# Kernel optimization log

Hardware: AMD Instinct MI355X
Metric: run time of the kernel (lower is better)

The kernel has to match this reference:

```python
import jax, jax.numpy as jnp
import numpy as np

EMBED_DIM = 1024
NUM_HEADS = 16
HEAD_DIM = EMBED_DIM // NUM_HEADS
SCALE = HEAD_DIM ** -0.5
BATCH, SEQ = 2, 2048


def setup_inputs() -> dict:
    key = jax.random.key(0)
    k1, k2, k3 = jax.random.split(key, 3)
    # Xavier-uniform-like init scales
    s_qkv = (6.0 / (3 * EMBED_DIM + EMBED_DIM)) ** 0.5
    s_out = (6.0 / (2 * EMBED_DIM)) ** 0.5
    return {
        "x": jax.random.normal(k1, (BATCH, SEQ, EMBED_DIM), dtype=jnp.float32),
        "w_qkv": jax.random.uniform(k2, (3 * EMBED_DIM, EMBED_DIM), jnp.float32, -s_qkv, s_qkv),
        "w_out": jax.random.uniform(k3, (EMBED_DIM, EMBED_DIM), jnp.float32, -s_out, s_out),
        "bias_qkv": jnp.zeros((3 * EMBED_DIM,), jnp.float32),
        "bias_out": jnp.zeros((EMBED_DIM,), jnp.float32),
    }


def reference(x, w_qkv, w_out, bias_qkv, bias_out):
    B, S, E = x.shape
    H, D = NUM_HEADS, HEAD_DIM
    # Fused QKV projection: [B,S,3E]
    qkv = jnp.einsum('bse,fe->bsf', x, w_qkv) + bias_qkv
    q, k, v = jnp.split(qkv, 3, axis=-1)
    # [B,H,S,D]
    q = q.reshape(B, S, H, D).transpose(0, 2, 1, 3)
    k = k.reshape(B, S, H, D).transpose(0, 2, 1, 3)
    v = v.reshape(B, S, H, D).transpose(0, 2, 1, 3)
    # Scaled dot-product attention (non-causal, no mask)
    scores = jnp.einsum('bhqd,bhkd->bhqk', q, k) * SCALE
    attn = jax.nn.softmax(scores, axis=-1)
    ctx = jnp.einsum('bhqk,bhkd->bhqd', attn, v)
    ctx = ctx.transpose(0, 2, 1, 3).reshape(B, S, E)
    # Output projection
    return jnp.einsum('bse,fe->bsf', ctx, w_out) + bias_out
```

## Files before the change

kernel.cpp:

```cpp
#include <hip/hip_runtime.h>
#include <stdint.h>

#define B_ 2
#define S_ 2048
#define E_ 1024
#define H_ 16
#define D_ 64
#define QSCALE_ 0.18033688011112042f

typedef __attribute__((ext_vector_type(4))) short short4_t;
typedef __attribute__((ext_vector_type(8))) short short8;
typedef __attribute__((ext_vector_type(2))) float f32x2;
typedef __attribute__((ext_vector_type(4))) float f32x4;
typedef __attribute__((ext_vector_type(16))) float f32x16;
typedef unsigned int u32;

__device__ __forceinline__ unsigned short f2bf(float x) {
    union { float f; u32 u; } v; v.f = x;
    u32 r = v.u + 0x7fffu + ((v.u >> 16) & 1u);
    return (unsigned short)(r >> 16);
}
__device__ __forceinline__ u32 fbits(float x) {
    union { float f; u32 u; } v; v.f = x; return v.u;
}
__device__ __forceinline__ u32 pkbf(float lo, float hi) {
    return __builtin_amdgcn_perm(fbits(hi), fbits(lo), 0x07060302u);
}

__device__ __forceinline__ f32x4 mfma16(short8 a, short8 b, f32x4 c) {
    return __builtin_amdgcn_mfma_f32_16x16x32_bf16(a, b, c, 0, 0, 0);
}
__device__ __forceinline__ f32x16 mfma32(short8 a, short8 b, f32x16 c) {
    return __builtin_amdgcn_mfma_f32_32x32x16_bf16(a, b, c, 0, 0, 0);
}

__device__ __forceinline__ void gld16(const unsigned short* g, unsigned short* l) {
    __builtin_amdgcn_global_load_lds(
        (const __attribute__((address_space(1))) u32*)g,
        (__attribute__((address_space(3))) u32*)l, 16, 0, 0);
}

__global__ __launch_bounds__(256) void cvt_kernel(
    const float* __restrict__ x, const float* __restrict__ wq,
    const float* __restrict__ wo,
    unsigned short* __restrict__ xb, unsigned short* __restrict__ wqb,
    unsigned short* __restrict__ wob)
{
    const long i8 = ((long)blockIdx.x * 256 + threadIdx.x) * 8;
    const float* src; unsigned short* dst; long off;
    if (i8 < 4194304)      { src = x;  dst = xb;  off = i8; }
    else if (i8 < 7340032) { src = wq; dst = wqb; off = i8 - 4194304; }
    else                   { src = wo; dst = wob; off = i8 - 7340032; }
    f32x4 a = *(const f32x4*)(src + off);
    f32x4 b = *(const f32x4*)(src + off + 4);
    short8 o;
    o[0] = (short)f2bf(a[0]); o[1] = (short)f2bf(a[1]);
    o[2] = (short)f2bf(a[2]); o[3] = (short)f2bf(a[3]);
    o[4] = (short)f2bf(b[0]); o[5] = (short)f2bf(b[1]);
    o[6] = (short)f2bf(b[2]); o[7] = (short)f2bf(b[3]);
    *(short8*)(dst + off) = o;
}

__global__ __launch_bounds__(256) void qkv_gemm_kernel(
    const unsigned short* __restrict__ x, const unsigned short* __restrict__ w,
    const float* __restrict__ bias,
    unsigned short* __restrict__ Qg, unsigned short* __restrict__ Kg,
    unsigned short* __restrict__ Vtg)
{
    __shared__ __attribute__((aligned(16))) unsigned char smem[16896];
    __shared__ float biass[128];
    unsigned short* As = (unsigned short*)smem;
    unsigned short* Bs = (unsigned short*)(smem + 8192);
    float* Tr = (float*)smem;

    const int t = threadIdx.x;
    const int m0 = blockIdx.x * 128;
    const int n0 = blockIdx.y * 128;
    const int lane = t & 63;
    const int wv = t >> 6;
    const int g = lane >> 4;
    const int l15 = lane & 15;
    const int wm = (wv >> 1) * 64;
    const int wn = (wv & 1) * 64;
    const int rloc = lane >> 2;
    const int cg = (lane & 3) ^ ((lane >> 3) & 3);
    const int rsw = (g ^ ((l15 >> 1) & 3)) * 8;

    if (t < 128) biass[t] = bias[n0 + t];

    f32x4 acc[4][4];
#pragma unroll
    for (int i = 0; i < 4; ++i)
#pragma unroll
        for (int j = 0; j < 4; ++j)
            acc[i][j] = (f32x4){0.f, 0.f, 0.f, 0.f};

    for (int kt = 0; kt < E_; kt += 32) {
        __syncthreads();
#pragma unroll
        for (int j = 0; j < 2; ++j) {
            const int rb = 32 * wv + 16 * j;
            gld16(x + (m0 + rb + rloc) * E_ + kt + cg * 8, &As[rb * 32]);
            gld16(w + (n0 + rb + rloc) * E_ + kt + cg * 8, &Bs[rb * 32]);
        }
        __syncthreads();

        short8 af[4], bf[4];
#pragma unroll
        for (int mt = 0; mt < 4; ++mt)
            af[mt] = *(const short8*)&As[(wm + mt * 16 + l15) * 32 + rsw];
#pragma unroll
        for (int nt = 0; nt < 4; ++nt)
            bf[nt] = *(const short8*)&Bs[(wn + nt * 16 + l15) * 32 + rsw];
#pragma unroll
        for (int mt = 0; mt < 4; ++mt)
#pragma unroll
            for (int nt = 0; nt < 4; ++nt)
                acc[mt][nt] = mfma16(af[mt], bf[nt], acc[mt][nt]);
    }

    if (n0 < 2048) {
#pragma unroll
        for (int mt = 0; mt < 4; ++mt) {
#pragma unroll
            for (int nt = 0; nt < 4; ++nt) {
                const int col = n0 + wn + nt * 16 + l15;
                const int which = col >> 10;
                const int cr = col & 1023;
                const int h = cr >> 6;
                const int d = cr & 63;
                const float bia = biass[col - n0];
#pragma unroll
                for (int i = 0; i < 4; ++i) {
                    const int row = m0 + wm + mt * 16 + g * 4 + i;
                    const int bb = row >> 11;
                    const int s = row & 2047;
                    const int bh = bb * H_ + h;
                    const float v = acc[mt][nt][i] + bia;
                    if (which == 0)
                        Qg[(bh * S_ + s) * D_ + d] = f2bf(v * QSCALE_);
                    else
                        Kg[(bh * S_ + s) * D_ + d] = f2bf(v);
                }
            }
        }
    } else {
        const int bb = m0 >> 11;
        const int s0 = m0 & 2047;
        const int dth = t >> 3;
        const int sc = t & 7;
#pragma unroll
        for (int sl = 0; sl < 4; ++sl) {
            __syncthreads();
            if ((wv & 1) == (sl >> 1)) {
#pragma unroll
                for (int q = 0; q < 2; ++q) {
                    const int nt = (sl & 1) * 2 + q;
                    const float bia = biass[wn + nt * 16 + l15];
                    const int dloc = q * 16 + l15;
#pragma unroll
                    for (int mt = 0; mt < 4; ++mt)
#pragma unroll
                        for (int i = 0; i < 4; ++i)
                            Tr[(wm + mt * 16 + g * 4 + i) * 33 + dloc] =
                                acc[mt][nt][i] + bia;
                }
            }
            __syncthreads();
            const int dglob = (n0 - 2048) + sl * 32 + dth;
            const int h = dglob >> 6;
            const int dd = dglob & 63;
            unsigned short* dst =
                Vtg + ((long)(bb * H_ + h) * D_ + dd) * S_ + s0 + sc * 16;
            short8 o0, o1;
#pragma unroll
            for (int j = 0; j < 8; ++j)
                o0[j] = (short)f2bf(Tr[(sc * 16 + j) * 33 + dth]);
#pragma unroll
            for (int j = 0; j < 8; ++j)
                o1[j] = (short)f2bf(Tr[(sc * 16 + 8 + j) * 33 + dth]);
            *(short8*)dst = o0;
            *(short8*)(dst + 8) = o1;
        }
    }
}

__global__ __launch_bounds__(128) void attn_kernel(
    const unsigned short* __restrict__ Qg, const unsigned short* __restrict__ Kg,
    const unsigned short* __restrict__ Vtg, unsigned short* __restrict__ ctx)
{
    __shared__ __attribute__((aligned(16))) unsigned short Ks[2][64 * 64];
    __shared__ __attribute__((aligned(16))) unsigned short Vs[2][64 * 64];
    __shared__ float lsumbuf[64];

    const int t = threadIdx.x;
    const int qb = blockIdx.x;
    const int bh = blockIdx.y;
    const int bb = bh >> 4;
    const int hh = bh & 15;
    const int lane = t & 63;
    const int wv = t >> 6;
    const int l31 = lane & 31;
    const int hf = lane >> 5;
    const int rloc = lane >> 3;
    const int cg = (lane & 7) ^ ((lane >> 3) & 7);
    const int sw = (l31 & 7);

    const int qrow0 = qb * 64 + wv * 32;
    short8 qa[4];
#pragma unroll
    for (int kc = 0; kc < 4; ++kc)
        qa[kc] = *(const short8*)(Qg + (bh * S_ + qrow0 + l31) * D_ + kc * 16 + hf * 8);

    const unsigned short* kp = Kg + (bh * S_ + 32 * wv + rloc) * D_ + cg * 8;
    const unsigned short* vp0 = Vtg + ((bh * D_ + 32 * wv + 0  + rloc) * S_) + cg * 8;
    const unsigned short* vp1 = Vtg + ((bh * D_ + 32 * wv + 8  + rloc) * S_) + cg * 8;
    const unsigned short* vp2 = Vtg + ((bh * D_ + 32 * wv + 16 + rloc) * S_) + cg * 8;
    const unsigned short* vp3 = Vtg + ((bh * D_ + 32 * wv + 24 + rloc) * S_) + cg * 8;

    f32x16 O[2];
    f32x2 lsum2 = (f32x2){0.f, 0.f};
#pragma unroll
    for (int r = 0; r < 16; ++r) { O[0][r] = 0.f; O[1][r] = 0.f; }

    auto stage = [&](int bufi) {
        unsigned short* kd = &Ks[bufi][(32 * wv) * 64];
        unsigned short* vd = &Vs[bufi][(32 * wv) * 64];
        gld16(kp,        kd);
        gld16(kp + 512,  kd + 512);
        gld16(kp + 1024, kd + 1024);
        gld16(kp + 1536, kd + 1536);
        gld16(vp0, vd);
        gld16(vp1, vd + 512);
        gld16(vp2, vd + 1024);
        gld16(vp3, vd + 1536);
    };
    auto advance = [&]() {
        kp += 64 * D_;
        vp0 += 64; vp1 += 64; vp2 += 64; vp3 += 64;
    };

    stage(0);
    advance();

    for (int kb = 0; kb < S_ / 64; ++kb) {
        __syncthreads();
        if (kb + 1 < S_ / 64) { stage((kb + 1) & 1); advance(); }
        const unsigned short* ks = Ks[kb & 1];
        const unsigned short* vs = Vs[kb & 1];

        f32x16 st[2];
#pragma unroll
        for (int kt = 0; kt < 2; ++kt) {
            f32x16 s;
#pragma unroll
            for (int r = 0; r < 16; ++r) s[r] = 0.f;
#pragma unroll
            for (int kc = 0; kc < 4; ++kc) {
                short8 kf = *(const short8*)&ks[(kt * 32 + l31) * 64 + ((2 * kc + hf) ^ sw) * 8];
                s = mfma32(kf, qa[kc], s);
            }
            st[kt] = s;
        }

#pragma unroll
        for (int kt = 0; kt < 2; ++kt) {
#pragma unroll
            for (int cp = 0; cp < 2; ++cp) {
                float p[8];
#pragma unroll
                for (int j = 0; j < 8; ++j)
                    p[j] = __builtin_amdgcn_exp2f(st[kt][8 * cp + j]);
                lsum2 += (f32x2){p[0], p[1]};
                lsum2 += (f32x2){p[2], p[3]};
                lsum2 += (f32x2){p[4], p[5]};
                lsum2 += (f32x2){p[6], p[7]};
                union { short8 s8; u32 u[4]; } pa;
                pa.u[0] = pkbf(p[0], p[1]);
                pa.u[1] = pkbf(p[2], p[3]);
                pa.u[2] = pkbf(p[4], p[5]);
                pa.u[3] = pkbf(p[6], p[7]);
                const int c0 = ((4 * kt + 2 * cp) ^ sw) * 8 + 4 * hf;
                const int c1 = ((4 * kt + 2 * cp + 1) ^ sw) * 8 + 4 * hf;
#pragma unroll
                for (int dt = 0; dt < 2; ++dt) {
                    short4_t v0 = *(const short4_t*)&vs[(dt * 32 + l31) * 64 + c0];
                    short4_t v1 = *(const short4_t*)&vs[(dt * 32 + l31) * 64 + c1];
                    short8 vb = __builtin_shufflevector(v0, v1, 0, 1, 2, 3, 4, 5, 6, 7);
                    O[dt] = mfma32(pa.s8, vb, O[dt]);
                }
            }
        }
    }

    float lsum = lsum2[0] + lsum2[1];
    lsum += __shfl_xor(lsum, 32);
    if (hf == 0) lsumbuf[wv * 32 + l31] = lsum;
    float inv[16];
#pragma unroll
    for (int r = 0; r < 16; ++r) {
        const int ql = wv * 32 + 4 * hf + (r & 3) + 8 * (r >> 2);
        inv[r] = 1.0f / lsumbuf[ql];
    }

#pragma unroll
    for (int dt = 0; dt < 2; ++dt)
#pragma unroll
        for (int r = 0; r < 16; ++r) {
            const int ql = wv * 32 + 4 * hf + (r & 3) + 8 * (r >> 2);
            const int s = qb * 64 + ql;
            ctx[(bb * S_ + s) * E_ + hh * D_ + dt * 32 + l31] = f2bf(O[dt][r] * inv[r]);
        }
}

__global__ __launch_bounds__(256) void out_gemm_kernel(
    const unsigned short* __restrict__ ctxg, const unsigned short* __restrict__ w,
    const float* __restrict__ bias, float* __restrict__ out)
{
    __shared__ __attribute__((aligned(16))) unsigned short As[128 * 32];
    __shared__ __attribute__((aligned(16))) unsigned short Bs[64 * 32];
    __shared__ float biass[64];

    const int t = threadIdx.x;
    const int m0 = blockIdx.x * 128;
    const int n0 = blockIdx.y * 64;
    const int lane = t & 63;
    const int wv = t >> 6;
    const int g = lane >> 4;
    const int l15 = lane & 15;
    const int wm = (wv >> 1) * 64;
    const int wn = (wv & 1) * 32;
    const int rloc = lane >> 2;
    const int cg = (lane & 3) ^ ((lane >> 3) & 3);
    const int rsw = (g ^ ((l15 >> 1) & 3)) * 8;

    if (t < 64) biass[t] = bias[n0 + t];

    f32x4 acc[4][2];
#pragma unroll
    for (int i = 0; i < 4; ++i)
#pragma unroll
        for (int j = 0; j < 2; ++j)
            acc[i][j] = (f32x4){0.f, 0.f, 0.f, 0.f};

    for (int kt = 0; kt < E_; kt += 32) {
        __syncthreads();
#pragma unroll
        for (int j = 0; j < 2; ++j) {
            const int rb = 32 * wv + 16 * j;
            gld16(ctxg + (m0 + rb + rloc) * E_ + kt + cg * 8, &As[rb * 32]);
        }
        {
            const int rb = 16 * wv;
            gld16(w + (n0 + rb + rloc) * E_ + kt + cg * 8, &Bs[rb * 32]);
        }
        __syncthreads();

        short8 af[4], bf[2];
#pragma unroll
        for (int mt = 0; mt < 4; ++mt)
            af[mt] = *(const short8*)&As[(wm + mt * 16 + l15) * 32 + rsw];
#pragma unroll
        for (int nt = 0; nt < 2; ++nt)
            bf[nt] = *(const short8*)&Bs[(wn + nt * 16 + l15) * 32 + rsw];
#pragma unroll
        for (int mt = 0; mt < 4; ++mt)
#pragma unroll
            for (int nt = 0; nt < 2; ++nt)
                acc[mt][nt] = mfma16(af[mt], bf[nt], acc[mt][nt]);
    }

#pragma unroll
    for (int mt = 0; mt < 4; ++mt) {
#pragma unroll
        for (int nt = 0; nt < 2; ++nt) {
            const int col = n0 + wn + nt * 16 + l15;
            const float bia = biass[col - n0];
#pragma unroll
            for (int i = 0; i < 4; ++i) {
                const int row = m0 + wm + mt * 16 + g * 4 + i;
                out[row * E_ + col] = acc[mt][nt][i] + bia;
            }
        }
    }
}

extern "C" void kernel_launch(void* const* d_in, const int* in_sizes, int n_in,
                              void* d_out, int out_size, void* d_ws, size_t ws_size,
                              hipStream_t stream) {
    const float* x    = (const float*)d_in[0];
    const float* wqkv = (const float*)d_in[1];
    const float* wout = (const float*)d_in[2];
    const float* bqkv = (const float*)d_in[3];
    const float* bout = (const float*)d_in[4];

    unsigned short* Q   = (unsigned short*)d_ws;
    unsigned short* K   = Q + 4194304;
    unsigned short* Vt  = K + 4194304;
    unsigned short* ctx = Vt + 4194304;
    unsigned short* xb  = ctx;
    unsigned short* wqb = ctx + 4194304;
    unsigned short* wob = wqb + 3145728;

    cvt_kernel<<<4096, 256, 0, stream>>>(x, wqkv, wout, xb, wqb, wob);
    qkv_gemm_kernel<<<dim3(32, 24), 256, 0, stream>>>(xb, wqb, bqkv, Q, K, Vt);
    attn_kernel<<<dim3(32, 32), 128, 0, stream>>>(Q, K, Vt, ctx);
    out_gemm_kernel<<<dim3(32, 16), 256, 0, stream>>>(ctx, wob, bout, (float*)d_out);
}
```

Before: 188.2 us.

## Use one wave per attention block computing 64 query rows with shared K/V fragments

The attention kernel now runs one 64-lane wave per block instead of two waves, and that wave handles both 32-row query halves. Each K and V fragment read from LDS is reused for two query tiles, which halves LDS fragment reads per MFMA, and V is read as a single short8 instead of two short4 loads. The cost is roughly double the registers per wave (two O accumulators and two Q sets) and fewer waves per CU to hide latency. Each stage now issues 16 global-to-LDS loads per lane, and a waitcnt(0) is added before every barrier. The QKV transpose store reorders element packing in a way that looks like it changes the output layout.

```diff
diff --git a/kernel.cpp b/kernel.cpp
--- a/kernel.cpp
+++ b/kernel.cpp
@@ -8,9 +8,7 @@
 #define D_ 64
 #define QSCALE_ 0.18033688011112042f
 
-typedef __attribute__((ext_vector_type(4))) short short4_t;
 typedef __attribute__((ext_vector_type(8))) short short8;
-typedef __attribute__((ext_vector_type(2))) float f32x2;
 typedef __attribute__((ext_vector_type(4))) float f32x4;
 typedef __attribute__((ext_vector_type(16))) float f32x16;
 typedef unsigned int u32;
@@ -174,18 +172,19 @@
                 Vtg + ((long)(bb * H_ + h) * D_ + dd) * S_ + s0 + sc * 16;
             short8 o0, o1;
 #pragma unroll
-            for (int j = 0; j < 8; ++j)
-                o0[j] = (short)f2bf(Tr[(sc * 16 + j) * 33 + dth]);
-#pragma unroll
-            for (int j = 0; j < 8; ++j)
-                o1[j] = (short)f2bf(Tr[(sc * 16 + 8 + j) * 33 + dth]);
+            for (int j = 0; j < 4; ++j) {
+                o0[j]     = (short)f2bf(Tr[(sc * 16 + j)      * 33 + dth]);
+                o0[4 + j] = (short)f2bf(Tr[(sc * 16 + 8 + j)  * 33 + dth]);
+                o1[j]     = (short)f2bf(Tr[(sc * 16 + 4 + j)  * 33 + dth]);
+                o1[4 + j] = (short)f2bf(Tr[(sc * 16 + 12 + j) * 33 + dth]);
+            }
             *(short8*)dst = o0;
             *(short8*)(dst + 8) = o1;
         }
     }
 }
 
-__global__ __launch_bounds__(128) void attn_kernel(
+__global__ __launch_bounds__(64, 1) void attn_kernel(
     const unsigned short* __restrict__ Qg, const unsigned short* __restrict__ Kg,
     const unsigned short* __restrict__ Vtg, unsigned short* __restrict__ ctx)
 {
@@ -193,124 +192,130 @@
     __shared__ __attribute__((aligned(16))) unsigned short Vs[2][64 * 64];
     __shared__ float lsumbuf[64];
 
-    const int t = threadIdx.x;
+    const int lane = threadIdx.x;
     const int qb = blockIdx.x;
     const int bh = blockIdx.y;
     const int bb = bh >> 4;
     const int hh = bh & 15;
-    const int lane = t & 63;
-    const int wv = t >> 6;
     const int l31 = lane & 31;
     const int hf = lane >> 5;
     const int rloc = lane >> 3;
     const int cg = (lane & 7) ^ ((lane >> 3) & 7);
-    const int sw = (l31 & 7);
-
-    const int qrow0 = qb * 64 + wv * 32;
-    short8 qa[4];
-#pragma unroll
-    for (int kc = 0; kc < 4; ++kc)
-        qa[kc] = *(const short8*)(Qg + (bh * S_ + qrow0 + l31) * D_ + kc * 16 + hf * 8);
-
-    const unsigned short* kp = Kg + (bh * S_ + 32 * wv + rloc) * D_ + cg * 8;
-    const unsigned short* vp0 = Vtg + ((bh * D_ + 32 * wv + 0  + rloc) * S_) + cg * 8;
-    const unsigned short* vp1 = Vtg + ((bh * D_ + 32 * wv + 8  + rloc) * S_) + cg * 8;
-    const unsigned short* vp2 = Vtg + ((bh * D_ + 32 * wv + 16 + rloc) * S_) + cg * 8;
-    const unsigned short* vp3 = Vtg + ((bh * D_ + 32 * wv + 24 + rloc) * S_) + cg * 8;
-
-    f32x16 O[2];
-    f32x2 lsum2 = (f32x2){0.f, 0.f};
-#pragma unroll
-    for (int r = 0; r < 16; ++r) { O[0][r] = 0.f; O[1][r] = 0.f; }
-
-    auto stage = [&](int bufi) {
-        unsigned short* kd = &Ks[bufi][(32 * wv) * 64];
-        unsigned short* vd = &Vs[bufi][(32 * wv) * 64];
-        gld16(kp,        kd);
-        gld16(kp + 512,  kd + 512);
-        gld16(kp + 1024, kd + 1024);
-        gld16(kp + 1536, kd + 1536);
-        gld16(vp0, vd);
-        gld16(vp1, vd + 512);
-        gld16(vp2, vd + 1024);
-        gld16(vp3, vd + 1536);
+    const int sw = l31 & 7;
+
+    short8 qa[2][4];
+#pragma unroll
+    for (int qh = 0; qh < 2; ++qh)
+#pragma unroll
+        for (int kc = 0; kc < 4; ++kc)
+            qa[qh][kc] = *(const short8*)(
+                Qg + (bh * S_ + qb * 64 + qh * 32 + l31) * D_ + kc * 16 + hf * 8);
+
+    f32x16 O[2][2];
+    float lsum[2] = {0.f, 0.f};
+#pragma unroll
+    for (int qh = 0; qh < 2; ++qh)
+#pragma unroll
+        for (int dt = 0; dt < 2; ++dt)
+#pragma unroll
+            for (int r = 0; r < 16; ++r) O[qh][dt][r] = 0.f;
+
+    auto stage = [&](int kb2, int bufi) {
+#pragma unroll
+        for (int i = 0; i < 8; ++i)
+            gld16(Kg + (bh * S_ + kb2 * 64 + i * 8 + rloc) * D_ + cg * 8,
+                  &Ks[bufi][i * 512]);
+#pragma unroll
+        for (int i = 0; i < 8; ++i)
+            gld16(Vtg + (bh * D_ + i * 8 + rloc) * S_ + kb2 * 64 + cg * 8,
+                  &Vs[bufi][i * 512]);
     };
-    auto advance = [&]() {
-        kp += 64 * D_;
-        vp0 += 64; vp1 += 64; vp2 += 64; vp3 += 64;
-    };
-
-    stage(0);
-    advance();
+
+    stage(0, 0);
 
     for (int kb = 0; kb < S_ / 64; ++kb) {
+        __builtin_amdgcn_s_waitcnt(0);
         __syncthreads();
-        if (kb + 1 < S_ / 64) { stage((kb + 1) & 1); advance(); }
+        if (kb + 1 < S_ / 64) stage(kb + 1, (kb + 1) & 1);
         const unsigned short* ks = Ks[kb & 1];
         const unsigned short* vs = Vs[kb & 1];
 
-        f32x16 st[2];
+        f32x16 st[2][2];
 #pragma unroll
         for (int kt = 0; kt < 2; ++kt) {
-            f32x16 s;
-#pragma unroll
-            for (int r = 0; r < 16; ++r) s[r] = 0.f;
-#pragma unroll
-            for (int kc = 0; kc < 4; ++kc) {
-                short8 kf = *(const short8*)&ks[(kt * 32 + l31) * 64 + ((2 * kc + hf) ^ sw) * 8];
-                s = mfma32(kf, qa[kc], s);
-            }
-            st[kt] = s;
+            short8 kf[4];
+#pragma unroll
+            for (int kc = 0; kc < 4; ++kc)
+                kf[kc] = *(const short8*)&ks[(kt * 32 + l31) * 64 + ((2 * kc + hf) ^ sw) * 8];
+#pragma unroll
+            for (int qh = 0; qh < 2; ++qh) {
+                f32x16 s;
+#pragma unroll
+                for (int r = 0; r < 16; ++r) s[r] = 0.f;
+#pragma unroll
+                for (int kc = 0; kc < 4; ++kc)
+                    s = mfma32(kf[kc], qa[qh][kc], s);
+                st[kt][qh] = s;
+            }
         }
 
 #pragma unroll
         for (int kt = 0; kt < 2; ++kt) {
 #pragma unroll
             for (int cp = 0; cp < 2; ++cp) {
-                float p[8];
-#pragma unroll
-                for (int j = 0; j < 8; ++j)
-                    p[j] = __builtin_amdgcn_exp2f(st[kt][8 * cp + j]);
-                lsum2 += (f32x2){p[0], p[1]};
-                lsum2 += (f32x2){p[2], p[3]};
-                lsum2 += (f32x2){p[4], p[5]};
-                lsum2 += (f32x2){p[6], p[7]};
-                union { short8 s8; u32 u[4]; } pa;
-                pa.u[0] = pkbf(p[0], p[1]);
-                pa.u[1] = pkbf(p[2], p[3]);
-                pa.u[2] = pkbf(p[4], p[5]);
-                pa.u[3] = pkbf(p[6], p[7]);
-                const int c0 = ((4 * kt + 2 * cp) ^ sw) * 8 + 4 * hf;
-                const int c1 = ((4 * kt + 2 * cp + 1) ^ sw) * 8 + 4 * hf;
-#pragma unroll
-                for (int dt = 0; dt < 2; ++dt) {
-                    short4_t v0 = *(const short4_t*)&vs[(dt * 32 + l31) * 64 + c0];
-                    short4_t v1 = *(const short4_t*)&vs[(dt * 32 + l31) * 64 + c1];
-                    short8 vb = __builtin_shufflevector(v0, v1, 0, 1, 2, 3, 4, 5, 6, 7);
-                    O[dt] = mfma32(pa.s8, vb, O[dt]);
+                short8 vb[2];
+#pragma unroll
+                for (int dt = 0; dt < 2; ++dt)
+                    vb[dt] = *(const short8*)&vs[(dt * 32 + l31) * 64 +
+                                                 ((4 * kt + 2 * cp + hf) ^ sw) * 8];
+#pragma unroll
+                for (int qh = 0; qh < 2; ++qh) {
+                    float p[8];
+#pragma unroll
+                    for (int j = 0; j < 8; ++j)
+                        p[j] = __builtin_amdgcn_exp2f(st[kt][qh][8 * cp + j]);
+                    lsum[qh] += (p[0] + p[1]) + (p[2] + p[3]) +
+                                (p[4] + p[5]) + (p[6] + p[7]);
+                    union { short8 s8; u32 u[4]; } pa;
+                    pa.u[0] = pkbf(p[0], p[1]);
+                    pa.u[1] = pkbf(p[2], p[3]);
+                    pa.u[2] = pkbf(p[4], p[5]);
+                    pa.u[3] = pkbf(p[6], p[7]);
+#pragma unroll
+                    for (int dt = 0; dt < 2; ++dt)
+                        O[qh][dt] = mfma32(pa.s8, vb[dt], O[qh][dt]);
                 }
             }
         }
     }
 
-    float lsum = lsum2[0] + lsum2[1];
-    lsum += __shfl_xor(lsum, 32);
-    if (hf == 0) lsumbuf[wv * 32 + l31] = lsum;
-    float inv[16];
-#pragma unroll
-    for (int r = 0; r < 16; ++r) {
-        const int ql = wv * 32 + 4 * hf + (r & 3) + 8 * (r >> 2);
-        inv[r] = 1.0f / lsumbuf[ql];
-    }
-
-#pragma unroll
-    for (int dt = 0; dt < 2; ++dt)
+#pragma unroll
+    for (int qh = 0; qh < 2; ++qh) {
+        float s = lsum[qh] + __shfl_xor(lsum[qh], 32);
+        if (hf == 0) lsumbuf[qh * 32 + l31] = s;
+    }
+    __builtin_amdgcn_s_waitcnt(0);
+    __syncthreads();
+    float inv[2][16];
+#pragma unroll
+    for (int qh = 0; qh < 2; ++qh)
 #pragma unroll
         for (int r = 0; r < 16; ++r) {
-            const int ql = wv * 32 + 4 * hf + (r & 3) + 8 * (r >> 2);
-            const int s = qb * 64 + ql;
-            ctx[(bb * S_ + s) * E_ + hh * D_ + dt * 32 + l31] = f2bf(O[dt][r] * inv[r]);
-        }
+            const int ql = qh * 32 + 4 * hf + (r & 3) + 8 * (r >> 2);
+            inv[qh][r] = 1.0f / lsumbuf[ql];
+        }
+
+#pragma unroll
+    for (int qh = 0; qh < 2; ++qh)
+#pragma unroll
+        for (int dt = 0; dt < 2; ++dt)
+#pragma unroll
+            for (int r = 0; r < 16; ++r) {
+                const int ql = qh * 32 + 4 * hf + (r & 3) + 8 * (r >> 2);
+                const int s = qb * 64 + ql;
+                ctx[(bb * S_ + s) * E_ + hh * D_ + dt * 32 + l31] =
+                    f2bf(O[qh][dt][r] * inv[qh][r]);
+            }
 }
 
 __global__ __launch_bounds__(256) void out_gemm_kernel(
@@ -404,6 +409,6 @@
 
     cvt_kernel<<<4096, 256, 0, stream>>>(x, wqkv, wout, xb, wqb, wob);
     qkv_gemm_kernel<<<dim3(32, 24), 256, 0, stream>>>(xb, wqb, bqkv, Q, K, Vt);
-    attn_kernel<<<dim3(32, 32), 128, 0, stream>>>(Q, K, Vt, ctx);
+    attn_kernel<<<dim3(32, 32), 64, 0, stream>>>(Q, K, Vt, ctx);
     out_gemm_kernel<<<dim3(32, 16), 256, 0, stream>>>(ctx, wob, bout, (float*)d_out);
 }
```

Result: no change. 191.2 us (+1.6%).
